# Performance work log

Measured on AMD Instinct MI355X. Metric: run time of the kernel, lower is better.

Reference implementation:

```python
import jax, jax.numpy as jnp
import numpy as np

D = 256        # emb_dim
H = 16         # num_heads
HD = D // H    # head_dim
N = 16384      # num users
B, S = 64, 128 # seq batch / length; M = B*S


def setup_inputs() -> dict:
    key = jax.random.key(0)
    ks = jax.random.split(key, 8)
    scale = 1.0 / np.sqrt(D)
    return {
        "user_feat": jax.random.normal(ks[0], (N, D), dtype=jnp.float32),
        "seq_feat": jax.random.normal(ks[1], (B, S, D), dtype=jnp.float32),
        "in_proj_w": jax.random.uniform(ks[2], (3 * D, D), jnp.float32, -scale, scale),
        "in_proj_b": jnp.zeros((3 * D,), jnp.float32),
        "out_proj_w": jax.random.uniform(ks[3], (D, D), jnp.float32, -scale, scale),
        "out_proj_b": jnp.zeros((D,), jnp.float32),
        "trans_w": jax.random.uniform(ks[4], (D, D), jnp.float32, -scale, scale),
        "trans_b": jax.random.uniform(ks[5], (D,), jnp.float32, -scale, scale),
    }


def _mha(x, in_proj_w, in_proj_b, out_proj_w, out_proj_b):
    # x: [B, S, D] self-attention, batch_first, like nn.MultiheadAttention
    qkv = jnp.einsum("bsd,ed->bse", x, in_proj_w) + in_proj_b  # [B,S,3D]
    q, k, v = jnp.split(qkv, 3, axis=-1)
    def heads(t):  # [B,S,D] -> [B,H,S,HD]
        return t.reshape(B, S, H, HD).transpose(0, 2, 1, 3)
    q, k, v = heads(q), heads(k), heads(v)
    scores = jnp.einsum("bhqd,bhkd->bhqk", q, k) / np.sqrt(HD)
    attn = jax.nn.softmax(scores, axis=-1)
    out = jnp.einsum("bhqk,bhkd->bhqd", attn, v)  # [B,H,S,HD]
    out = out.transpose(0, 2, 1, 3).reshape(B, S, D)
    return out @ out_proj_w.T + out_proj_b


def reference(user_feat, seq_feat, in_proj_w, in_proj_b, out_proj_w, out_proj_b, trans_w, trans_b):
    seq = _mha(seq_feat, in_proj_w, in_proj_b, out_proj_w, out_proj_b)
    seq = seq.reshape(-1, D)                        # [M, D]
    M = seq.shape[0]
    att = user_feat @ seq.T                         # [N, M]
    att = att / jnp.maximum(jnp.sum(jnp.abs(att), axis=1, keepdims=True), 1e-12)  # F.normalize p=1
    # mean_j Linear(att_ij * seq_j) == Linear((att @ seq) / M)  (exact, by linearity)
    agg = (att @ seq) / M                           # [N, D]
    return user_feat + (agg @ trans_w.T + trans_b)
```

## Files before the change

kernel.cpp:

```cpp
#include <hip/hip_runtime.h>


typedef __bf16 bf16_t;
typedef __bf16 bf16x8 __attribute__((ext_vector_type(8)));
typedef __bf16 bf16x4 __attribute__((ext_vector_type(4)));
typedef float  f32x4  __attribute__((ext_vector_type(4)));
typedef unsigned int u32x4 __attribute__((ext_vector_type(4)));

#define MFMA16(a, b, c) __builtin_amdgcn_mfma_f32_16x16x32_bf16((a), (b), (c), 0, 0, 0)

#define AS1 __attribute__((address_space(1)))
#define AS3 __attribute__((address_space(3)))
#define GLOAD_LDS16(g, l) \
    __builtin_amdgcn_global_load_lds((const AS1 unsigned int*)(const void*)(g), \
                                     (AS3 unsigned int*)(void*)(l), 16, 0, 0)

__device__ __forceinline__ int swz256(int row, int k) { return row * 256 + (k ^ ((row & 7) << 3)); }

__global__ void k_cvt_all(const float* __restrict__ x, const float* __restrict__ w1,
                          const float* __restrict__ w2,
                          bf16_t* __restrict__ xb, bf16_t* __restrict__ w1b,
                          bf16_t* __restrict__ w2b) {
    const int NX = 8192 * 256 / 4, NW1 = 768 * 256 / 4, NW2 = 256 * 256 / 4;
    const int total = NX + NW1 + NW2;
    int i  = blockIdx.x * blockDim.x + threadIdx.x;
    int st = gridDim.x * blockDim.x;
    for (; i < total; i += st) {
        const float* s; bf16_t* d; int k;
        if (i < NX)            { s = x;  d = xb;  k = i; }
        else if (i < NX + NW1) { s = w1; d = w1b; k = i - NX; }
        else                   { s = w2; d = w2b; k = i - NX - NW1; }
        float4 v = ((const float4*)s)[k];
        bf16x4 o = { (bf16_t)v.x, (bf16_t)v.y, (bf16_t)v.z, (bf16_t)v.w };
        ((bf16x4*)d)[k] = o;
    }
}

__global__ __launch_bounds__(256, 1)
void k_gemm_bt(const bf16_t* __restrict__ A, const bf16_t* __restrict__ B,
               const float* __restrict__ bias, bf16_t* __restrict__ Cb, int N) {
    __shared__ bf16_t Al[64 * 256];
    __shared__ bf16_t Bl[64 * 256];
    const int tid  = threadIdx.x;
    const int lane = tid & 63;
    const int w    = tid >> 6;
    const int l15  = lane & 15;
    const int l4   = lane >> 4;
    const int rb = blockIdx.y * 64, cb = blockIdx.x * 64;

    {
        const u32x4* sa = (const u32x4*)(A + (size_t)rb * 256);
        const u32x4* sb = (const u32x4*)(B + (size_t)cb * 256);
        u32x4* da = (u32x4*)Al;
        u32x4* db = (u32x4*)Bl;
#pragma unroll
        for (int i = 0; i < 8; ++i) {
            int ch  = i * 256 + tid;
            int row = ch >> 5, cp = ch & 31;
            int sch = (ch & ~31) | (cp ^ (row & 7));
            da[sch] = sa[ch];
            db[sch] = sb[ch];
        }
    }
    __syncthreads();

    f32x4 acc[4];
#pragma unroll
    for (int n = 0; n < 4; ++n) acc[n] = (f32x4){0.f, 0.f, 0.f, 0.f};
#pragma unroll
    for (int t = 0; t < 8; ++t) {
        int k = t * 32 + l4 * 8;
        bf16x8 af = *(const bf16x8*)(Al + swz256(16 * w + l15, k));
#pragma unroll
        for (int n = 0; n < 4; ++n) {
            bf16x8 bfr = *(const bf16x8*)(Bl + swz256(16 * n + l15, k));
            acc[n] = MFMA16(af, bfr, acc[n]);
        }
    }
#pragma unroll
    for (int n = 0; n < 4; ++n) {
        int col = cb + 16 * n + l15;
        float bv = bias ? bias[col] : 0.f;
#pragma unroll
        for (int r = 0; r < 4; ++r) {
            int row = rb + 16 * w + l4 * 4 + r;
            Cb[(size_t)row * N + col] = (bf16_t)(acc[n][r] + bv);
        }
    }
}

__global__ __launch_bounds__(256, 1)
void k_gemm_seqT(const bf16_t* __restrict__ A, const bf16_t* __restrict__ B,
                 const float* __restrict__ bias, bf16_t* __restrict__ Cb,
                 bf16_t* __restrict__ CTb) {
    __shared__ bf16_t Al[64 * 256];
    __shared__ bf16_t Bl[64 * 256];
    __shared__ float  Tt[64][65];
    const int tid  = threadIdx.x;
    const int lane = tid & 63;
    const int w    = tid >> 6;
    const int l15  = lane & 15;
    const int l4   = lane >> 4;
    const int rb = blockIdx.y * 64, cb = blockIdx.x * 64;

    {
        const u32x4* sa = (const u32x4*)(A + (size_t)rb * 256);
        const u32x4* sb = (const u32x4*)(B + (size_t)cb * 256);
        u32x4* da = (u32x4*)Al;
        u32x4* db = (u32x4*)Bl;
#pragma unroll
        for (int i = 0; i < 8; ++i) {
            int ch  = i * 256 + tid;
            int row = ch >> 5, cp = ch & 31;
            int sch = (ch & ~31) | (cp ^ (row & 7));
            da[sch] = sa[ch];
            db[sch] = sb[ch];
        }
    }
    __syncthreads();

    f32x4 acc[4];
#pragma unroll
    for (int n = 0; n < 4; ++n) acc[n] = (f32x4){0.f, 0.f, 0.f, 0.f};
#pragma unroll
    for (int t = 0; t < 8; ++t) {
        int k = t * 32 + l4 * 8;
        bf16x8 af = *(const bf16x8*)(Al + swz256(16 * w + l15, k));
#pragma unroll
        for (int n = 0; n < 4; ++n) {
            bf16x8 bfr = *(const bf16x8*)(Bl + swz256(16 * n + l15, k));
            acc[n] = MFMA16(af, bfr, acc[n]);
        }
    }
#pragma unroll
    for (int n = 0; n < 4; ++n) {
        int col = cb + 16 * n + l15;
        float bv = bias[col];
#pragma unroll
        for (int r = 0; r < 4; ++r) {
            int row = rb + 16 * w + l4 * 4 + r;
            float v = acc[n][r] + bv;
            Cb[(size_t)row * 256 + col] = (bf16_t)v;
            Tt[16 * n + l15][16 * w + l4 * 4 + r] = v;
        }
    }
    __syncthreads();
#pragma unroll
    for (int i = 0; i < 16; ++i) {
        int e = i * 256 + tid;
        int lc = e >> 6, lr = e & 63;
        CTb[(size_t)(cb + lc) * 8192 + rb + lr] = (bf16_t)Tt[lc][lr];
    }
}

__global__ __launch_bounds__(128, 1)
void k_mha(const bf16_t* __restrict__ qkv, bf16_t* __restrict__ attn) {
    __shared__ float Kl[128][17];
    __shared__ float Vl[128][17];
    const int bh = blockIdx.x;
    const int b = bh >> 4, h = bh & 15;
    const int t = threadIdx.x;
    const size_t rowbase = (size_t)b * 128;

    const bf16_t* base = qkv + (rowbase + t) * 768 + h * 16;
    bf16x8 qa = *(const bf16x8*)(base),       qb = *(const bf16x8*)(base + 8);
    bf16x8 ka = *(const bf16x8*)(base + 256), kb = *(const bf16x8*)(base + 264);
    bf16x8 va = *(const bf16x8*)(base + 512), vb = *(const bf16x8*)(base + 520);
    float q[16];
#pragma unroll
    for (int e = 0; e < 8; ++e) {
        q[e] = (float)qa[e]; q[8 + e] = (float)qb[e];
        Kl[t][e] = (float)ka[e]; Kl[t][8 + e] = (float)kb[e];
        Vl[t][e] = (float)va[e]; Vl[t][8 + e] = (float)vb[e];
    }
    __syncthreads();

    float m = -1e30f;
    for (int j = 0; j < 128; ++j) {
        float s = 0.f;
#pragma unroll
        for (int d = 0; d < 16; ++d) s += q[d] * Kl[j][d];
        m = fmaxf(m, s * 0.25f);
    }
    float sum = 0.f;
    float o[16];
#pragma unroll
    for (int d = 0; d < 16; ++d) o[d] = 0.f;
    for (int j = 0; j < 128; ++j) {
        float s = 0.f;
#pragma unroll
        for (int d = 0; d < 16; ++d) s += q[d] * Kl[j][d];
        float e = __expf(s * 0.25f - m);
        sum += e;
#pragma unroll
        for (int d = 0; d < 16; ++d) o[d] += e * Vl[j][d];
    }
    float inv = 1.f / sum;
    bf16_t* out = attn + (rowbase + t) * 256 + h * 16;
#pragma unroll
    for (int d = 0; d < 16; ++d) out[d] = (bf16_t)(o[d] * inv);
}

__global__ __launch_bounds__(512, 1)
void k_rowabs(const float* __restrict__ Uf, const bf16_t* __restrict__ Sq,
              float* __restrict__ rsp) {
    __shared__ bf16_t Kl[3][64 * 256];

    const int tid  = threadIdx.x;
    const int lane = tid & 63;
    const int wid  = tid >> 6;
    const int wr   = wid >> 2;
    const int wc   = wid & 3;
    const int l15  = lane & 15;
    const int l4   = lane >> 4;
    const int q0   = blockIdx.x * 128;
    const int jy   = blockIdx.y;
    const int jbase = jy * 4096;
    const int NT   = 64;

    int koff[4];
#pragma unroll
    for (int i = 0; i < 4; ++i) {
        int c = wid * 256 + i * 64 + lane;
        int sc = (c & ~31) | ((c & 31) ^ ((c >> 5) & 7));
        koff[i] = sc * 16;
    }
    auto stage = [&](int b, int j0) {
        const char* gK = (const char*)Sq + (size_t)j0 * 512;
        char* lK = (char*)(&Kl[b][0]) + wid * 4096;
#pragma unroll
        for (int i = 0; i < 4; ++i) GLOAD_LDS16(gK + koff[i], lK + i * 1024);
    };

    bf16x8 uf[4][8];
#pragma unroll
    for (int rt = 0; rt < 4; ++rt) {
        const float* up = Uf + (size_t)(q0 + 64 * wr + 16 * rt + l15) * 256 + l4 * 8;
#pragma unroll
        for (int t = 0; t < 8; ++t) {
            float4 fa = *(const float4*)(up + t * 32);
            float4 fb = *(const float4*)(up + t * 32 + 4);
            bf16x8 v = { (bf16_t)fa.x, (bf16_t)fa.y, (bf16_t)fa.z, (bf16_t)fa.w,
                         (bf16_t)fb.x, (bf16_t)fb.y, (bf16_t)fb.z, (bf16_t)fb.w };
            uf[rt][t] = v;
        }
    }

    float rsacc[4][4];
#pragma unroll
    for (int rt = 0; rt < 4; ++rt)
#pragma unroll
        for (int r = 0; r < 4; ++r) rsacc[rt][r] = 0.f;

    stage(0, jbase);
    stage(1, jbase + 64);

    int cur = 0;
    for (int it = 0; it < NT; ++it) {
        if (it + 1 < NT) asm volatile("s_waitcnt vmcnt(4)" ::: "memory");
        else             asm volatile("s_waitcnt vmcnt(0)" ::: "memory");
        __builtin_amdgcn_s_barrier();
        __builtin_amdgcn_sched_barrier(0);
        if (it + 2 < NT) {
            int nb = cur + 2; if (nb >= 3) nb -= 3;
            stage(nb, jbase + (it + 2) * 64);
        }

        const bf16_t* Klc = &Kl[cur][0];
        f32x4 sacc[4];
#pragma unroll
        for (int rt = 0; rt < 4; ++rt) sacc[rt] = (f32x4){0.f, 0.f, 0.f, 0.f};
#pragma unroll
        for (int t = 0; t < 8; ++t) {
            int k = t * 32 + l4 * 8;
            bf16x8 bfr = *(const bf16x8*)(Klc + swz256(16 * wc + l15, k));
#pragma unroll
            for (int rt = 0; rt < 4; ++rt)
                sacc[rt] = MFMA16(uf[rt][t], bfr, sacc[rt]);
        }
#pragma unroll
        for (int rt = 0; rt < 4; ++rt)
#pragma unroll
            for (int r = 0; r < 4; ++r) rsacc[rt][r] += fabsf(sacc[rt][r]);

        ++cur; if (cur >= 3) cur = 0;
    }

    float* rdst = rsp + (size_t)(jy * 4 + wc) * 16384 + q0 + 64 * wr;
#pragma unroll
    for (int rt = 0; rt < 4; ++rt)
#pragma unroll
        for (int r = 0; r < 4; ++r) {
            float v = rsacc[rt][r];
            v += __shfl_xor(v, 1, 16);
            v += __shfl_xor(v, 2, 16);
            v += __shfl_xor(v, 4, 16);
            v += __shfl_xor(v, 8, 16);
            if (l15 == 0) rdst[16 * rt + 4 * l4 + r] = v;
        }
}

__global__ __launch_bounds__(256, 1)
void k_gram(const bf16_t* __restrict__ ST, float* __restrict__ Gpart) {
    __shared__ bf16_t Al[64 * 256];
    __shared__ bf16_t Bl[64 * 256];
    const int tid = threadIdx.x, lane = tid & 63, w = tid >> 6;
    const int l15 = lane & 15, l4 = lane >> 4;
    const int rb = blockIdx.y * 64, cb = blockIdx.x * 64;
    const int jb = blockIdx.z * 1024;

    f32x4 acc[4];
#pragma unroll
    for (int n = 0; n < 4; ++n) acc[n] = (f32x4){0.f, 0.f, 0.f, 0.f};

    for (int kt4 = 0; kt4 < 4; ++kt4) {
        int j0 = jb + kt4 * 256;
        __syncthreads();
        u32x4* da = (u32x4*)Al;
        u32x4* db = (u32x4*)Bl;
#pragma unroll
        for (int i = 0; i < 8; ++i) {
            int ch  = i * 256 + tid;
            int row = ch >> 5, cp = ch & 31;
            int sch = (ch & ~31) | (cp ^ (row & 7));
            da[sch] = *(const u32x4*)(ST + (size_t)(rb + row) * 8192 + j0 + cp * 8);
            db[sch] = *(const u32x4*)(ST + (size_t)(cb + row) * 8192 + j0 + cp * 8);
        }
        __syncthreads();
#pragma unroll
        for (int t = 0; t < 8; ++t) {
            int k = t * 32 + l4 * 8;
            bf16x8 af = *(const bf16x8*)(Al + swz256(16 * w + l15, k));
#pragma unroll
            for (int n = 0; n < 4; ++n) {
                bf16x8 bfr = *(const bf16x8*)(Bl + swz256(16 * n + l15, k));
                acc[n] = MFMA16(af, bfr, acc[n]);
            }
        }
    }
    float* gp = Gpart + (size_t)blockIdx.z * 65536;
#pragma unroll
    for (int n = 0; n < 4; ++n)
#pragma unroll
        for (int r = 0; r < 4; ++r)
            gp[(size_t)(rb + 16 * w + l4 * 4 + r) * 256 + cb + 16 * n + l15] = acc[n][r];
}

__global__ __launch_bounds__(256, 1)
void k_gh(const float* __restrict__ Gpart, const float* __restrict__ W,
          bf16_t* __restrict__ HT) {
    __shared__ bf16_t Al[64 * 256];
    __shared__ bf16_t Bl[64 * 256];
    const int tid = threadIdx.x, lane = tid & 63, w = tid >> 6;
    const int l15 = lane & 15, l4 = lane >> 4;
    const int rb = blockIdx.y * 64, cb = blockIdx.x * 64;

#pragma unroll
    for (int i = 0; i < 16; ++i) {
        int idx = i * 1024 + tid * 4;
        int row = idx >> 8, col = idx & 255;
        f32x4 s = *(const f32x4*)(Gpart + (size_t)(rb + row) * 256 + col);
#pragma unroll
        for (int p = 1; p < 8; ++p)
            s += *(const f32x4*)(Gpart + (size_t)p * 65536 + (size_t)(rb + row) * 256 + col);
        f32x4 wv = *(const f32x4*)(W + (size_t)(cb + row) * 256 + col);
        int sc = col ^ ((row & 7) << 3);
        bf16x4 ga = { (bf16_t)s[0], (bf16_t)s[1], (bf16_t)s[2], (bf16_t)s[3] };
        bf16x4 wb = { (bf16_t)wv[0], (bf16_t)wv[1], (bf16_t)wv[2], (bf16_t)wv[3] };
        *(bf16x4*)(Al + row * 256 + sc) = ga;
        *(bf16x4*)(Bl + row * 256 + sc) = wb;
    }
    __syncthreads();

    f32x4 acc[4];
#pragma unroll
    for (int n = 0; n < 4; ++n) acc[n] = (f32x4){0.f, 0.f, 0.f, 0.f};
#pragma unroll
    for (int t = 0; t < 8; ++t) {
        int k = t * 32 + l4 * 8;
        bf16x8 af = *(const bf16x8*)(Al + swz256(16 * w + l15, k));
#pragma unroll
        for (int n = 0; n < 4; ++n) {
            bf16x8 bfr = *(const bf16x8*)(Bl + swz256(16 * n + l15, k));
            acc[n] = MFMA16(af, bfr, acc[n]);
        }
    }
#pragma unroll
    for (int n = 0; n < 4; ++n)
#pragma unroll
        for (int r = 0; r < 4; ++r)
            HT[(size_t)(cb + 16 * n + l15) * 256 + rb + 16 * w + l4 * 4 + r] =
                (bf16_t)acc[n][r];
}

__global__ __launch_bounds__(256, 1)
void k_final(const float* __restrict__ user, const bf16_t* __restrict__ B,
             const float* __restrict__ rsp, const float* __restrict__ tb,
             float* __restrict__ out) {
    __shared__ bf16_t Al[64 * 256];
    __shared__ bf16_t Bl[64 * 256];
    __shared__ float  crs[64];
    const int tid  = threadIdx.x;
    const int lane = tid & 63;
    const int w    = tid >> 6;
    const int l15  = lane & 15;
    const int l4   = lane >> 4;
    const int rb = blockIdx.y * 64, cb = blockIdx.x * 64;

    {
        const u32x4* sb = (const u32x4*)(B + (size_t)cb * 256);
        u32x4* db = (u32x4*)Bl;
#pragma unroll
        for (int i = 0; i < 8; ++i) {
            int ch  = i * 256 + tid;
            int row = ch >> 5, cp = ch & 31;
            int sch = (ch & ~31) | (cp ^ (row & 7));
            const float* up = user + (size_t)(rb + row) * 256 + cp * 8;
            float4 fa = *(const float4*)up;
            float4 fb = *(const float4*)(up + 4);
            bf16x8 v = { (bf16_t)fa.x, (bf16_t)fa.y, (bf16_t)fa.z, (bf16_t)fa.w,
                         (bf16_t)fb.x, (bf16_t)fb.y, (bf16_t)fb.z, (bf16_t)fb.w };
            *(bf16x8*)(Al + sch * 8) = v;
            db[sch] = sb[ch];
        }
    }
    if (tid < 64) {
        float s = 0.f;
#pragma unroll
        for (int p = 0; p < 8; ++p) s += rsp[(size_t)p * 16384 + rb + tid];
        crs[tid] = 1.f / (fmaxf(s, 1e-12f) * 8192.f);
    }
    __syncthreads();

    f32x4 acc[4];
#pragma unroll
    for (int n = 0; n < 4; ++n) acc[n] = (f32x4){0.f, 0.f, 0.f, 0.f};
#pragma unroll
    for (int t = 0; t < 8; ++t) {
        int k = t * 32 + l4 * 8;
        bf16x8 af = *(const bf16x8*)(Al + swz256(16 * w + l15, k));
#pragma unroll
        for (int n = 0; n < 4; ++n) {
            bf16x8 bfr = *(const bf16x8*)(Bl + swz256(16 * n + l15, k));
            acc[n] = MFMA16(af, bfr, acc[n]);
        }
    }
    float c[4];
#pragma unroll
    for (int r = 0; r < 4; ++r) c[r] = crs[16 * w + l4 * 4 + r];
#pragma unroll
    for (int n = 0; n < 4; ++n) {
        int col = cb + 16 * n + l15;
        float bv = tb[col];
#pragma unroll
        for (int r = 0; r < 4; ++r) {
            int row = rb + 16 * w + l4 * 4 + r;
            size_t idx = (size_t)row * 256 + col;
            out[idx] = user[idx] + c[r] * acc[n][r] + bv;
        }
    }
}

extern "C" void kernel_launch(void* const* d_in, const int* in_sizes, int n_in,
                              void* d_out, int out_size, void* d_ws, size_t ws_size,
                              hipStream_t stream) {
    const float* user_feat  = (const float*)d_in[0];
    const float* seq_feat   = (const float*)d_in[1];
    const float* in_proj_w  = (const float*)d_in[2];
    const float* in_proj_b  = (const float*)d_in[3];
    const float* out_proj_w = (const float*)d_in[4];
    const float* out_proj_b = (const float*)d_in[5];
    const float* trans_w    = (const float*)d_in[6];
    const float* trans_b    = (const float*)d_in[7];
    float* out = (float*)d_out;

    char* w = (char*)d_ws;
    size_t off = 0;
    auto take = [&](size_t bytes) { void* p = w + off; off += (bytes + 255) & ~(size_t)255; return p; };
    bf16_t* Xb    = (bf16_t*)take((size_t)8192 * 256 * 2);
    bf16_t* W1b   = (bf16_t*)take((size_t)768 * 256 * 2);
    bf16_t* W2b   = (bf16_t*)take((size_t)256 * 256 * 2);
    bf16_t* attnb = (bf16_t*)take((size_t)8192 * 256 * 2);
    bf16_t* seqb  = (bf16_t*)take((size_t)8192 * 256 * 2);
    bf16_t* seqTb = (bf16_t*)take((size_t)256 * 8192 * 2);
    char*   regA  = (char*)take((size_t)8192 * 768 * 4);
    bf16_t* qkvb  = (bf16_t*)regA;
    float*  Gpart = (float*)regA;
    bf16_t* HTb   = (bf16_t*)(regA + (size_t)8 * 65536 * 4);
    float*  rsp   = (float*)Xb;

    k_cvt_all<<<1024, 256, 0, stream>>>(seq_feat, in_proj_w, out_proj_w, Xb, W1b, W2b);

    k_gemm_bt<<<dim3(12, 128), 256, 0, stream>>>(Xb, W1b, in_proj_b, qkvb, 768);

    k_mha<<<1024, 128, 0, stream>>>(qkvb, attnb);

    k_gemm_seqT<<<dim3(4, 128), 256, 0, stream>>>(attnb, W2b, out_proj_b, seqb, seqTb);

    k_rowabs<<<dim3(128, 2), 512, 0, stream>>>(user_feat, seqb, rsp);

    k_gram<<<dim3(4, 4, 8), 256, 0, stream>>>(seqTb, Gpart);
    k_gh<<<dim3(4, 4), 256, 0, stream>>>(Gpart, trans_w, HTb);

    k_final<<<dim3(4, 256), 256, 0, stream>>>(user_feat, HTb, rsp, trans_b, out);
}
```

Before: 188.1 us.

## Fuse fp32-to-bf16 conversion into GEMM loads and restructure rowabs pipeline

Removes the standalone conversion kernel. The QKV and out-proj GEMMs now read fp32 inputs and weights and convert to bf16 while staging into LDS. The rowabs kernel changes from a 3-stage async pipeline with partial waits to a double buffer of two 64-row tiles per iteration with full __syncthreads. Several kernels also get launch_bounds raised to 2 blocks per CU. This saves one launch and the bf16 intermediate round-trip, but GEMM loads double in bytes, and the coarser syncs in rowabs may expose more load latency.

```diff
diff --git a/kernel.cpp b/kernel.cpp
--- a/kernel.cpp
+++ b/kernel.cpp
@@ -17,28 +17,17 @@
 
 __device__ __forceinline__ int swz256(int row, int k) { return row * 256 + (k ^ ((row & 7) << 3)); }
 
-__global__ void k_cvt_all(const float* __restrict__ x, const float* __restrict__ w1,
-                          const float* __restrict__ w2,
-                          bf16_t* __restrict__ xb, bf16_t* __restrict__ w1b,
-                          bf16_t* __restrict__ w2b) {
-    const int NX = 8192 * 256 / 4, NW1 = 768 * 256 / 4, NW2 = 256 * 256 / 4;
-    const int total = NX + NW1 + NW2;
-    int i  = blockIdx.x * blockDim.x + threadIdx.x;
-    int st = gridDim.x * blockDim.x;
-    for (; i < total; i += st) {
-        const float* s; bf16_t* d; int k;
-        if (i < NX)            { s = x;  d = xb;  k = i; }
-        else if (i < NX + NW1) { s = w1; d = w1b; k = i - NX; }
-        else                   { s = w2; d = w2b; k = i - NX - NW1; }
-        float4 v = ((const float4*)s)[k];
-        bf16x4 o = { (bf16_t)v.x, (bf16_t)v.y, (bf16_t)v.z, (bf16_t)v.w };
-        ((bf16x4*)d)[k] = o;
-    }
-}
-
-__global__ __launch_bounds__(256, 1)
-void k_gemm_bt(const bf16_t* __restrict__ A, const bf16_t* __restrict__ B,
-               const float* __restrict__ bias, bf16_t* __restrict__ Cb, int N) {
+__device__ __forceinline__ bf16x8 cvt8(const float* p) {
+    float4 fa = *(const float4*)p;
+    float4 fb = *(const float4*)(p + 4);
+    bf16x8 v = { (bf16_t)fa.x, (bf16_t)fa.y, (bf16_t)fa.z, (bf16_t)fa.w,
+                 (bf16_t)fb.x, (bf16_t)fb.y, (bf16_t)fb.z, (bf16_t)fb.w };
+    return v;
+}
+
+__global__ __launch_bounds__(256, 2)
+void k_gemm_f32(const float* __restrict__ A, const float* __restrict__ B,
+                const float* __restrict__ bias, bf16_t* __restrict__ Cb, int N) {
     __shared__ bf16_t Al[64 * 256];
     __shared__ bf16_t Bl[64 * 256];
     const int tid  = threadIdx.x;
@@ -49,17 +38,13 @@
     const int rb = blockIdx.y * 64, cb = blockIdx.x * 64;
 
     {
-        const u32x4* sa = (const u32x4*)(A + (size_t)rb * 256);
-        const u32x4* sb = (const u32x4*)(B + (size_t)cb * 256);
-        u32x4* da = (u32x4*)Al;
-        u32x4* db = (u32x4*)Bl;
 #pragma unroll
         for (int i = 0; i < 8; ++i) {
             int ch  = i * 256 + tid;
             int row = ch >> 5, cp = ch & 31;
             int sch = (ch & ~31) | (cp ^ (row & 7));
-            da[sch] = sa[ch];
-            db[sch] = sb[ch];
+            *(bf16x8*)(Al + sch * 8) = cvt8(A + (size_t)(rb + row) * 256 + cp * 8);
+            *(bf16x8*)(Bl + sch * 8) = cvt8(B + (size_t)(cb + row) * 256 + cp * 8);
         }
     }
     __syncthreads();
@@ -80,7 +65,7 @@
 #pragma unroll
     for (int n = 0; n < 4; ++n) {
         int col = cb + 16 * n + l15;
-        float bv = bias ? bias[col] : 0.f;
+        float bv = bias[col];
 #pragma unroll
         for (int r = 0; r < 4; ++r) {
             int row = rb + 16 * w + l4 * 4 + r;
@@ -90,7 +75,7 @@
 }
 
 __global__ __launch_bounds__(256, 1)
-void k_gemm_seqT(const bf16_t* __restrict__ A, const bf16_t* __restrict__ B,
+void k_gemm_seqT(const bf16_t* __restrict__ A, const float* __restrict__ B,
                  const float* __restrict__ bias, bf16_t* __restrict__ Cb,
                  bf16_t* __restrict__ CTb) {
     __shared__ bf16_t Al[64 * 256];
@@ -105,16 +90,14 @@
 
     {
         const u32x4* sa = (const u32x4*)(A + (size_t)rb * 256);
-        const u32x4* sb = (const u32x4*)(B + (size_t)cb * 256);
         u32x4* da = (u32x4*)Al;
-        u32x4* db = (u32x4*)Bl;
 #pragma unroll
         for (int i = 0; i < 8; ++i) {
             int ch  = i * 256 + tid;
             int row = ch >> 5, cp = ch & 31;
             int sch = (ch & ~31) | (cp ^ (row & 7));
             da[sch] = sa[ch];
-            db[sch] = sb[ch];
+            *(bf16x8*)(Bl + sch * 8) = cvt8(B + (size_t)(cb + row) * 256 + cp * 8);
         }
     }
     __syncthreads();
@@ -204,7 +187,7 @@
 __global__ __launch_bounds__(512, 1)
 void k_rowabs(const float* __restrict__ Uf, const bf16_t* __restrict__ Sq,
               float* __restrict__ rsp) {
-    __shared__ bf16_t Kl[3][64 * 256];
+    __shared__ bf16_t Kl[2][2][64 * 256];
 
     const int tid  = threadIdx.x;
     const int lane = tid & 63;
@@ -216,7 +199,7 @@
     const int q0   = blockIdx.x * 128;
     const int jy   = blockIdx.y;
     const int jbase = jy * 4096;
-    const int NT   = 64;
+    const int NT   = 32;
 
     int koff[4];
 #pragma unroll
@@ -225,9 +208,9 @@
         int sc = (c & ~31) | ((c & 31) ^ ((c >> 5) & 7));
         koff[i] = sc * 16;
     }
-    auto stage = [&](int b, int j0) {
+    auto stage = [&](int b, int h, int j0) {
         const char* gK = (const char*)Sq + (size_t)j0 * 512;
-        char* lK = (char*)(&Kl[b][0]) + wid * 4096;
+        char* lK = (char*)(&Kl[b][h][0]) + wid * 4096;
 #pragma unroll
         for (int i = 0; i < 4; ++i) GLOAD_LDS16(gK + koff[i], lK + i * 1024);
     };
@@ -237,13 +220,7 @@
     for (int rt = 0; rt < 4; ++rt) {
         const float* up = Uf + (size_t)(q0 + 64 * wr + 16 * rt + l15) * 256 + l4 * 8;
 #pragma unroll
-        for (int t = 0; t < 8; ++t) {
-            float4 fa = *(const float4*)(up + t * 32);
-            float4 fb = *(const float4*)(up + t * 32 + 4);
-            bf16x8 v = { (bf16_t)fa.x, (bf16_t)fa.y, (bf16_t)fa.z, (bf16_t)fa.w,
-                         (bf16_t)fb.x, (bf16_t)fb.y, (bf16_t)fb.z, (bf16_t)fb.w };
-            uf[rt][t] = v;
-        }
+        for (int t = 0; t < 8; ++t) uf[rt][t] = cvt8(up + t * 32);
     }
 
     float rsacc[4][4];
@@ -252,38 +229,36 @@
 #pragma unroll
         for (int r = 0; r < 4; ++r) rsacc[rt][r] = 0.f;
 
-    stage(0, jbase);
-    stage(1, jbase + 64);
-
-    int cur = 0;
+    stage(0, 0, jbase);
+    stage(0, 1, jbase + 64);
+    __syncthreads();
+
     for (int it = 0; it < NT; ++it) {
-        if (it + 1 < NT) asm volatile("s_waitcnt vmcnt(4)" ::: "memory");
-        else             asm volatile("s_waitcnt vmcnt(0)" ::: "memory");
-        __builtin_amdgcn_s_barrier();
-        __builtin_amdgcn_sched_barrier(0);
-        if (it + 2 < NT) {
-            int nb = cur + 2; if (nb >= 3) nb -= 3;
-            stage(nb, jbase + (it + 2) * 64);
-        }
-
-        const bf16_t* Klc = &Kl[cur][0];
-        f32x4 sacc[4];
-#pragma unroll
-        for (int rt = 0; rt < 4; ++rt) sacc[rt] = (f32x4){0.f, 0.f, 0.f, 0.f};
-#pragma unroll
-        for (int t = 0; t < 8; ++t) {
-            int k = t * 32 + l4 * 8;
-            bf16x8 bfr = *(const bf16x8*)(Klc + swz256(16 * wc + l15, k));
+        const int cur = it & 1;
+        if (it + 1 < NT) {
+            stage(cur ^ 1, 0, jbase + (it + 1) * 128);
+            stage(cur ^ 1, 1, jbase + (it + 1) * 128 + 64);
+        }
+#pragma unroll
+        for (int hh = 0; hh < 2; ++hh) {
+            const bf16_t* Klc = &Kl[cur][hh][0];
+            f32x4 sacc[4];
+#pragma unroll
+            for (int rt = 0; rt < 4; ++rt) sacc[rt] = (f32x4){0.f, 0.f, 0.f, 0.f};
+#pragma unroll
+            for (int t = 0; t < 8; ++t) {
+                int k = t * 32 + l4 * 8;
+                bf16x8 bfr = *(const bf16x8*)(Klc + swz256(16 * wc + l15, k));
+#pragma unroll
+                for (int rt = 0; rt < 4; ++rt)
+                    sacc[rt] = MFMA16(uf[rt][t], bfr, sacc[rt]);
+            }
 #pragma unroll
             for (int rt = 0; rt < 4; ++rt)
-                sacc[rt] = MFMA16(uf[rt][t], bfr, sacc[rt]);
-        }
-#pragma unroll
-        for (int rt = 0; rt < 4; ++rt)
-#pragma unroll
-            for (int r = 0; r < 4; ++r) rsacc[rt][r] += fabsf(sacc[rt][r]);
-
-        ++cur; if (cur >= 3) cur = 0;
+#pragma unroll
+                for (int r = 0; r < 4; ++r) rsacc[rt][r] += fabsf(sacc[rt][r]);
+        }
+        __syncthreads();
     }
 
     float* rdst = rsp + (size_t)(jy * 4 + wc) * 16384 + q0 + 64 * wr;
@@ -300,7 +275,7 @@
         }
 }
 
-__global__ __launch_bounds__(256, 1)
+__global__ __launch_bounds__(256, 2)
 void k_gram(const bf16_t* __restrict__ ST, float* __restrict__ Gpart) {
     __shared__ bf16_t Al[64 * 256];
     __shared__ bf16_t Bl[64 * 256];
@@ -346,7 +321,7 @@
             gp[(size_t)(rb + 16 * w + l4 * 4 + r) * 256 + cb + 16 * n + l15] = acc[n][r];
 }
 
-__global__ __launch_bounds__(256, 1)
+__global__ __launch_bounds__(256, 2)
 void k_gh(const float* __restrict__ Gpart, const float* __restrict__ W,
           bf16_t* __restrict__ HT) {
     __shared__ bf16_t Al[64 * 256];
@@ -393,7 +368,7 @@
                 (bf16_t)acc[n][r];
 }
 
-__global__ __launch_bounds__(256, 1)
+__global__ __launch_bounds__(256, 2)
 void k_final(const float* __restrict__ user, const bf16_t* __restrict__ B,
              const float* __restrict__ rsp, const float* __restrict__ tb,
              float* __restrict__ out) {
@@ -415,12 +390,7 @@
             int ch  = i * 256 + tid;
             int row = ch >> 5, cp = ch & 31;
             int sch = (ch & ~31) | (cp ^ (row & 7));
-            const float* up = user + (size_t)(rb + row) * 256 + cp * 8;
-            float4 fa = *(const float4*)up;
-            float4 fb = *(const float4*)(up + 4);
-            bf16x8 v = { (bf16_t)fa.x, (bf16_t)fa.y, (bf16_t)fa.z, (bf16_t)fa.w,
-                         (bf16_t)fb.x, (bf16_t)fb.y, (bf16_t)fb.z, (bf16_t)fb.w };
-            *(bf16x8*)(Al + sch * 8) = v;
+            *(bf16x8*)(Al + sch * 8) = cvt8(user + (size_t)(rb + row) * 256 + cp * 8);
             db[sch] = sb[ch];
         }
     }
@@ -477,25 +447,20 @@
     char* w = (char*)d_ws;
     size_t off = 0;
     auto take = [&](size_t bytes) { void* p = w + off; off += (bytes + 255) & ~(size_t)255; return p; };
-    bf16_t* Xb    = (bf16_t*)take((size_t)8192 * 256 * 2);
-    bf16_t* W1b   = (bf16_t*)take((size_t)768 * 256 * 2);
-    bf16_t* W2b   = (bf16_t*)take((size_t)256 * 256 * 2);
     bf16_t* attnb = (bf16_t*)take((size_t)8192 * 256 * 2);
     bf16_t* seqb  = (bf16_t*)take((size_t)8192 * 256 * 2);
     bf16_t* seqTb = (bf16_t*)take((size_t)256 * 8192 * 2);
+    float*  rsp   = (float*)take((size_t)8 * 16384 * 4);
     char*   regA  = (char*)take((size_t)8192 * 768 * 4);
     bf16_t* qkvb  = (bf16_t*)regA;
     float*  Gpart = (float*)regA;
     bf16_t* HTb   = (bf16_t*)(regA + (size_t)8 * 65536 * 4);
-    float*  rsp   = (float*)Xb;
-
-    k_cvt_all<<<1024, 256, 0, stream>>>(seq_feat, in_proj_w, out_proj_w, Xb, W1b, W2b);
-
-    k_gemm_bt<<<dim3(12, 128), 256, 0, stream>>>(Xb, W1b, in_proj_b, qkvb, 768);
+
+    k_gemm_f32<<<dim3(12, 128), 256, 0, stream>>>(seq_feat, in_proj_w, in_proj_b, qkvb, 768);
 
     k_mha<<<1024, 128, 0, stream>>>(qkvb, attnb);
 
-    k_gemm_seqT<<<dim3(4, 128), 256, 0, stream>>>(attnb, W2b, out_proj_b, seqb, seqTb);
+    k_gemm_seqT<<<dim3(4, 128), 256, 0, stream>>>(attnb, out_proj_w, out_proj_b, seqb, seqTb);
 
     k_rowabs<<<dim3(128, 2), 512, 0, stream>>>(user_feat, seqb, rsp);
 
```

Result: faster. 182.6 us (-2.9%).
